# Kernel tuning notes

Measured on AMD Instinct MI355X. Metric: run time of the kernel, lower is better.

The kernel has to match this reference:

```python
import jax, jax.numpy as jnp
import numpy as np
import math

N_EMBD = 1024
N_HEAD = 16
HEAD_DIM = N_EMBD // N_HEAD
SEQ = 2048
BATCH = 2
EPS = 1e-5


def _gelu_tanh(x):
    c = math.sqrt(2.0 / math.pi)
    return 0.5 * x * (1.0 + jnp.tanh(c * (x + 0.044715 * x ** 3)))


def _layernorm(x, w, b):
    mean = jnp.mean(x, axis=-1, keepdims=True)
    var = jnp.mean(jnp.square(x - mean), axis=-1, keepdims=True)  # unbiased=False
    return (x - mean) / jnp.sqrt(var + EPS) * w + b


def setup_inputs() -> dict:
    key = jax.random.key(0)
    ks = jax.random.split(key, 8)
    D = N_EMBD
    s = 0.02
    return {
        "x": jax.random.normal(ks[0], (BATCH, SEQ, D), jnp.float32),
        "ln1_w": jnp.ones((D,), jnp.float32),
        "ln1_b": jnp.zeros((D,), jnp.float32),
        "w_qkv": jax.random.normal(ks[1], (D, 3 * D), jnp.float32) * s,
        "b_qkv": jnp.zeros((3 * D,), jnp.float32),
        "w_attn_proj": jax.random.normal(ks[2], (D, D), jnp.float32) * s,
        "b_attn_proj": jnp.zeros((D,), jnp.float32),
        "ln2_w": jnp.ones((D,), jnp.float32),
        "ln2_b": jnp.zeros((D,), jnp.float32),
        "w_fc": jax.random.normal(ks[3], (D, 4 * D), jnp.float32) * s,
        "b_fc": jnp.zeros((4 * D,), jnp.float32),
        "w_proj": jax.random.normal(ks[4], (4 * D, D), jnp.float32) * s,
        "b_proj": jnp.zeros((D,), jnp.float32),
    }


def reference(x, ln1_w, ln1_b, w_qkv, b_qkv, w_attn_proj, b_attn_proj,
              ln2_w, ln2_b, w_fc, b_fc, w_proj, b_proj):
    bs, T, D = x.shape
    # --- attention branch (pre-LN) ---
    h = _layernorm(x, ln1_w, ln1_b)
    qkv = h @ w_qkv + b_qkv                      # [B,T,3D]
    q, k, v = jnp.split(qkv, 3, axis=-1)
    q = q.reshape(bs, T, N_HEAD, HEAD_DIM).transpose(0, 2, 1, 3)  # [B,H,T,d]
    k = k.reshape(bs, T, N_HEAD, HEAD_DIM).transpose(0, 2, 1, 3)
    v = v.reshape(bs, T, N_HEAD, HEAD_DIM).transpose(0, 2, 1, 3)
    scores = jnp.einsum("bhqd,bhkd->bhqk", q, k) * (1.0 / math.sqrt(HEAD_DIM))
    causal = jnp.tril(jnp.ones((T, T), bool))
    scores = jnp.where(causal[None, None], scores, -jnp.inf)
    att = jax.nn.softmax(scores, axis=-1)
    ctx = jnp.einsum("bhqk,bhkd->bhqd", att, v)
    ctx = ctx.transpose(0, 2, 1, 3).reshape(bs, T, D)
    attn_out = ctx @ w_attn_proj + b_attn_proj
    x = x + attn_out
    # --- MLP branch (pre-LN) ---
    h = _layernorm(x, ln2_w, ln2_b)
    h = _gelu_tanh(h @ w_fc + b_fc)
    h = h @ w_proj + b_proj
    return x + h
```

## Files before the change

kernel.cpp:

```cpp
#include <hip/hip_runtime.h>

typedef unsigned short u16;
typedef __attribute__((ext_vector_type(8))) __bf16 bf16x8;
typedef __attribute__((ext_vector_type(8))) unsigned short ushort8;
typedef __attribute__((ext_vector_type(4))) float f32x4;

#define MFMA16(a, b, c) __builtin_amdgcn_mfma_f32_16x16x32_bf16((a), (b), (c), 0, 0, 0)

__device__ __forceinline__ u16 f2bf(float f) {
  union { float f; unsigned u; } v; v.f = f;
  unsigned r = v.u + 0x7fffu + ((v.u >> 16) & 1u);
  return (u16)(r >> 16);
}

__device__ __forceinline__ void async16(const u16* g, u16* l) {
  __builtin_amdgcn_global_load_lds(
      (const __attribute__((address_space(1))) void*)g,
      (__attribute__((address_space(3))) void*)l, 16, 0, 0);
}

__global__ __launch_bounds__(256)
void transpose_bf16(const float* __restrict__ W, u16* __restrict__ Wt, int K, int N) {
  __shared__ float t[32][33];
  const int n0 = blockIdx.x * 32, k0 = blockIdx.y * 32;
  const int tx = threadIdx.x, ty = threadIdx.y;
  #pragma unroll
  for (int i = 0; i < 32; i += 8)
    t[ty + i][tx] = W[(size_t)(k0 + ty + i) * N + n0 + tx];
  __syncthreads();
  #pragma unroll
  for (int i = 0; i < 32; i += 8)
    Wt[(size_t)(n0 + ty + i) * K + k0 + tx] = f2bf(t[tx][ty + i]);
}

__global__ __launch_bounds__(256)
void transpose_v(const u16* __restrict__ v, u16* __restrict__ vt) {
  __shared__ u16 t[64][72];
  const int bh = blockIdx.y, t0 = blockIdx.x * 64;
  const int tid = threadIdx.x;
  #pragma unroll
  for (int s = 0; s < 2; ++s) {
    const int idx = tid + s * 256;
    const int row = idx >> 3, ch = idx & 7;
    ushort8 d = *(const ushort8*)(v + ((size_t)bh * 2048 + t0 + row) * 64 + ch * 8);
    #pragma unroll
    for (int e = 0; e < 8; ++e) t[ch * 8 + e][row] = d[e];
  }
  __syncthreads();
  #pragma unroll
  for (int s = 0; s < 2; ++s) {
    const int idx = tid + s * 256;
    const int drow = idx >> 3, ch = idx & 7;
    ushort8 o = *(const ushort8*)(&t[drow][ch * 8]);
    *(ushort8*)(vt + ((size_t)bh * 64 + drow) * 2048 + t0 + ch * 8) = o;
  }
}

__global__ __launch_bounds__(256)
void ln_bf16(const float* __restrict__ X, const float* __restrict__ w,
             const float* __restrict__ bia, u16* __restrict__ out) {
  const int row = blockIdx.x, tid = threadIdx.x;
  const float4 v = ((const float4*)(X + (size_t)row * 1024))[tid];
  float s = v.x + v.y + v.z + v.w;
  float s2 = v.x * v.x + v.y * v.y + v.z * v.z + v.w * v.w;
  #pragma unroll
  for (int o = 32; o > 0; o >>= 1) { s += __shfl_down(s, o); s2 += __shfl_down(s2, o); }
  __shared__ float red[8];
  const int wv = tid >> 6, lane = tid & 63;
  if (lane == 0) { red[wv] = s; red[4 + wv] = s2; }
  __syncthreads();
  s = red[0] + red[1] + red[2] + red[3];
  s2 = red[4] + red[5] + red[6] + red[7];
  const float mean = s * (1.f / 1024.f);
  const float var = s2 * (1.f / 1024.f) - mean * mean;
  const float rstd = rsqrtf(var + 1e-5f);
  const float4 wv4 = ((const float4*)w)[tid];
  const float4 bv4 = ((const float4*)bia)[tid];
  ushort4 o;
  o.x = f2bf((v.x - mean) * rstd * wv4.x + bv4.x);
  o.y = f2bf((v.y - mean) * rstd * wv4.y + bv4.y);
  o.z = f2bf((v.z - mean) * rstd * wv4.z + bv4.z);
  o.w = f2bf((v.w - mean) * rstd * wv4.w + bv4.w);
  ((ushort4*)(out + (size_t)row * 1024))[tid] = o;
}

template <int MODE>
__global__ __launch_bounds__(256)
void gemm_bt(const u16* __restrict__ A, const u16* __restrict__ Bt,
             const float* __restrict__ bias, const float* __restrict__ resid,
             float* __restrict__ outF, u16* __restrict__ outB,
             u16* __restrict__ qo, u16* __restrict__ ko, u16* __restrict__ vo,
             int M, int N, int K, int kSlice) {
  __shared__ u16 As[128 * 64];
  __shared__ u16 Bs[128 * 64];
  const int tid = threadIdx.x;
  const int lane = tid & 63, wv = tid >> 6;
  const int l16 = lane & 15, quad = lane >> 4;
  const int wr = wv >> 1, wc = wv & 1;
  const int m0 = blockIdx.y * 128, n0 = blockIdx.x * 128;
  const int kBegin = blockIdx.z * kSlice, kEnd = kBegin + kSlice;
  const int srow = lane >> 3;
  const int sch = (lane & 7) ^ srow;

  f32x4 acc[4][4];
  const f32x4 fz = {0.f, 0.f, 0.f, 0.f};
  #pragma unroll
  for (int i = 0; i < 4; ++i)
    #pragma unroll
    for (int j = 0; j < 4; ++j) acc[i][j] = fz;

  for (int k0 = kBegin; k0 < kEnd; k0 += 64) {
    __syncthreads();
    #pragma unroll
    for (int s = 0; s < 4; ++s) {
      const int R = wv * 32 + s * 8;
      async16(A + (size_t)(m0 + R + srow) * K + k0 + sch * 8, As + R * 64);
      async16(Bt + (size_t)(n0 + R + srow) * K + k0 + sch * 8, Bs + R * 64);
    }
    __builtin_amdgcn_s_waitcnt(0xF70);
    __syncthreads();
    #pragma unroll
    for (int h = 0; h < 2; ++h) {
      bf16x8 af[4], bfr[4];
      #pragma unroll
      for (int i = 0; i < 4; ++i) {
        const int row = wr * 64 + i * 16 + l16;
        af[i] = *(const bf16x8*)(As + row * 64 + (((h * 4 + quad) ^ (l16 & 7)) * 8));
      }
      #pragma unroll
      for (int j = 0; j < 4; ++j) {
        const int row = wc * 64 + j * 16 + l16;
        bfr[j] = *(const bf16x8*)(Bs + row * 64 + (((h * 4 + quad) ^ (l16 & 7)) * 8));
      }
      #pragma unroll
      for (int i = 0; i < 4; ++i)
        #pragma unroll
        for (int j = 0; j < 4; ++j)
          acc[i][j] = MFMA16(af[i], bfr[j], acc[i][j]);
    }
  }

  #pragma unroll
  for (int i = 0; i < 4; ++i) {
    #pragma unroll
    for (int j = 0; j < 4; ++j) {
      const int col = n0 + wc * 64 + j * 16 + l16;
      const float bc = bias[col];
      #pragma unroll
      for (int r = 0; r < 4; ++r) {
        const int row = m0 + wr * 64 + i * 16 + quad * 4 + r;
        float v = acc[i][j][r];
        if (MODE != 4) v += bc;
        if (MODE == 0) {
          const int which = col >> 10, cc = col & 1023, hh = cc >> 6, dd = cc & 63;
          const int bb = row >> 11, t = row & 2047;
          const u16 bv = f2bf(v);
          const size_t o = ((size_t)(bb * 16 + hh) * 2048 + t) * 64 + dd;
          if (which == 0)
            qo[o] = bv;
          else if (which == 1)
            ko[o] = bv;
          else
            vo[o] = bv;
        } else if (MODE == 1) {
          outF[(size_t)row * N + col] = resid[(size_t)row * N + col] + v;
        } else if (MODE == 2) {
          const float x3 = v * v * v;
          const float u = 0.7978845608028654f * (v + 0.044715f * x3);
          const float e = __expf(2.f * u);
          const float th = 1.f - 2.f / (e + 1.f);
          outB[(size_t)row * N + col] = f2bf(0.5f * v * (1.f + th));
        } else {
          outF[(size_t)blockIdx.z * M * N + (size_t)row * N + col] = v;
        }
      }
    }
  }
}

__global__ __launch_bounds__(256)
void reduce2(const float* __restrict__ P, const float* __restrict__ resid,
             const float* __restrict__ bias, float* __restrict__ out, int MN, int N) {
  const int idx4 = blockIdx.x * 256 + threadIdx.x;
  const size_t s = (size_t)MN >> 2;
  const float4 a = ((const float4*)P)[idx4];
  const float4 b = ((const float4*)P)[idx4 + s];
  const float4 r = ((const float4*)resid)[idx4];
  const float4 bb = ((const float4*)bias)[idx4 & (N / 4 - 1)];
  float4 o;
  o.x = r.x + a.x + b.x + bb.x;
  o.y = r.y + a.y + b.y + bb.y;
  o.z = r.z + a.z + b.z + bb.z;
  o.w = r.w + a.w + b.w + bb.w;
  ((float4*)out)[idx4] = o;
}

__global__ __launch_bounds__(256)
void attn(const u16* __restrict__ Q, const u16* __restrict__ Kg,
          const u16* __restrict__ Vt, u16* __restrict__ ctx) {
  __shared__ u16 Ks[128 * 64];
  __shared__ u16 Vs[64 * 128];
  __shared__ u16 Ps[64 * 128];
  const int px = blockIdx.x;
  const int pair = px >> 1, half = px & 1;
  const int qt0 = pair, qt1 = 15 - pair;
  const int bh = blockIdx.y;
  const int b = bh >> 4, h = bh & 15;
  const int tid = threadIdx.x;
  const int lane = tid & 63, wv = tid >> 6;
  const int l16 = lane & 15, quad = lane >> 4;
  const int rb = half * 64 + wv * 16;
  const u16* Qb = Q + (size_t)bh * 2048 * 64;
  const u16* Kb = Kg + (size_t)bh * 2048 * 64;
  const u16* Vb = Vt + (size_t)bh * 64 * 2048;

  bf16x8 qf[2][2];
  #pragma unroll
  for (int t = 0; t < 2; ++t)
    #pragma unroll
    for (int c = 0; c < 2; ++c)
      qf[t][c] = *(const bf16x8*)(Qb + (size_t)((t ? qt1 : qt0) * 128 + rb + l16) * 64 +
                                  c * 32 + quad * 8);

  f32x4 octx[2][4];
  const f32x4 fz = {0.f, 0.f, 0.f, 0.f};
  #pragma unroll
  for (int t = 0; t < 2; ++t)
    #pragma unroll
    for (int jd = 0; jd < 4; ++jd) octx[t][jd] = fz;
  float mi[2][4], li[2][4];
  #pragma unroll
  for (int t = 0; t < 2; ++t)
    #pragma unroll
    for (int r = 0; r < 4; ++r) { mi[t][r] = -1e30f; li[t][r] = 0.f; }

  for (int kt = 0; kt <= qt1; ++kt) {
    __syncthreads();
    #pragma unroll
    for (int s = 0; s < 4; ++s) {
      const int cid = tid + s * 256;
      {
        const int key = cid >> 3, ch = cid & 7;
        ushort8 d = *(const ushort8*)(Kb + (size_t)(kt * 128 + key) * 64 + ch * 8);
        *(ushort8*)(Ks + key * 64 + ((ch ^ (key & 7)) * 8)) = d;
      }
      {
        const int dd = cid >> 4, ch = cid & 15;
        ushort8 d = *(const ushort8*)(Vb + (size_t)dd * 2048 + kt * 128 + ch * 8);
        *(ushort8*)(Vs + dd * 128 + ((ch ^ (dd & 15)) * 8)) = d;
      }
    }
    __syncthreads();

    #pragma unroll
    for (int t = 0; t < 2; ++t) {
      const int qt = t ? qt1 : qt0;
      if (kt > qt) continue;

      f32x4 sa[8];
      #pragma unroll
      for (int j = 0; j < 8; ++j) {
        const int key7 = l16 & 7;
        bf16x8 kf0 = *(const bf16x8*)(Ks + (16 * j + l16) * 64 + ((quad ^ key7) * 8));
        bf16x8 kf1 = *(const bf16x8*)(Ks + (16 * j + l16) * 64 + (((4 + quad) ^ key7) * 8));
        f32x4 tt = MFMA16(qf[t][0], kf0, fz);
        sa[j] = MFMA16(qf[t][1], kf1, tt);
      }
      if (kt == qt) {
        #pragma unroll
        for (int j = 0; j < 8; ++j)
          #pragma unroll
          for (int r = 0; r < 4; ++r) {
            const int rg = rb + quad * 4 + r;
            const int cg = j * 16 + l16;
            if (cg > rg) sa[j][r] = -1e30f;
          }
      }
      #pragma unroll
      for (int r = 0; r < 4; ++r) {
        float mx = -1e30f;
        #pragma unroll
        for (int j = 0; j < 8; ++j) mx = fmaxf(mx, sa[j][r]);
        mx = fmaxf(mx, __shfl_xor(mx, 1));
        mx = fmaxf(mx, __shfl_xor(mx, 2));
        mx = fmaxf(mx, __shfl_xor(mx, 4));
        mx = fmaxf(mx, __shfl_xor(mx, 8));
        mx *= 0.125f;
        const float mn = fmaxf(mi[t][r], mx);
        const float al = __expf(mi[t][r] - mn);
        mi[t][r] = mn;
        const int row = wv * 16 + quad * 4 + r;
        const int rl = row & 15;
        float rs = 0.f;
        #pragma unroll
        for (int j = 0; j < 8; ++j) {
          const float p = __expf(sa[j][r] * 0.125f - mn);
          rs += p;
          const int colc = 2 * j + (l16 >> 3);
          Ps[row * 128 + ((colc ^ rl) * 8) + (l16 & 7)] = f2bf(p);
        }
        rs += __shfl_xor(rs, 1);
        rs += __shfl_xor(rs, 2);
        rs += __shfl_xor(rs, 4);
        rs += __shfl_xor(rs, 8);
        li[t][r] = li[t][r] * al + rs;
        #pragma unroll
        for (int jd = 0; jd < 4; ++jd) octx[t][jd][r] *= al;
      }
      #pragma unroll
      for (int c = 0; c < 4; ++c) {
        const int row = wv * 16 + l16;
        bf16x8 pf = *(const bf16x8*)(Ps + row * 128 + (((c * 4 + quad) ^ l16) * 8));
        #pragma unroll
        for (int jd = 0; jd < 4; ++jd) {
          const int dd = jd * 16 + l16;
          bf16x8 vf = *(const bf16x8*)(Vs + dd * 128 + (((c * 4 + quad) ^ (dd & 15)) * 8));
          octx[t][jd] = MFMA16(pf, vf, octx[t][jd]);
        }
      }
    }
  }
  #pragma unroll
  for (int t = 0; t < 2; ++t) {
    const int qt = t ? qt1 : qt0;
    #pragma unroll
    for (int jd = 0; jd < 4; ++jd)
      #pragma unroll
      for (int r = 0; r < 4; ++r) {
        const int rowg = qt * 128 + rb + quad * 4 + r;
        const int col = h * 64 + jd * 16 + l16;
        ctx[((size_t)b * 2048 + rowg) * 1024 + col] = f2bf(octx[t][jd][r] / li[t][r]);
      }
  }
}

extern "C" void kernel_launch(void* const* d_in, const int* in_sizes, int n_in,
                              void* d_out, int out_size, void* d_ws, size_t ws_size,
                              hipStream_t stream) {
  (void)in_sizes; (void)n_in; (void)out_size; (void)ws_size;
  const float* x      = (const float*)d_in[0];
  const float* ln1_w  = (const float*)d_in[1];
  const float* ln1_b  = (const float*)d_in[2];
  const float* w_qkv  = (const float*)d_in[3];
  const float* b_qkv  = (const float*)d_in[4];
  const float* w_attn = (const float*)d_in[5];
  const float* b_attn = (const float*)d_in[6];
  const float* ln2_w  = (const float*)d_in[7];
  const float* ln2_b  = (const float*)d_in[8];
  const float* w_fc   = (const float*)d_in[9];
  const float* b_fc   = (const float*)d_in[10];
  const float* w_proj = (const float*)d_in[11];
  const float* b_proj = (const float*)d_in[12];
  float* out = (float*)d_out;

  char* ws = (char*)d_ws;
  size_t off = 0;
  auto alloc = [&](size_t n) {
    char* p = ws + off;
    off += (n + 255) & ~(size_t)255;
    return p;
  };
  u16* h1     = (u16*)alloc(4096ull * 1024 * 2);
  u16* wqkvT  = (u16*)alloc(3072ull * 1024 * 2);
  u16* wattnT = (u16*)alloc(1024ull * 1024 * 2);
  u16* wfcT   = (u16*)alloc(4096ull * 1024 * 2);
  u16* wprojT = (u16*)alloc(1024ull * 4096 * 2);
  u16* q      = (u16*)alloc(4096ull * 1024 * 2);
  u16* k      = (u16*)alloc(4096ull * 1024 * 2);
  u16* vT     = (u16*)alloc(4096ull * 1024 * 2);
  u16* ctxb   = (u16*)alloc(4096ull * 1024 * 2);
  float* out1 = (float*)alloc(4096ull * 1024 * 4);
  u16* h2     = (u16*)alloc(4096ull * 1024 * 2);
  u16* fco    = (u16*)alloc(4096ull * 4096 * 2);

  u16* vtmp = ctxb;
  float* projP = (float*)q;

  const dim3 tb(32, 8);
  transpose_bf16<<<dim3(3072 / 32, 1024 / 32), tb, 0, stream>>>(w_qkv, wqkvT, 1024, 3072);
  transpose_bf16<<<dim3(1024 / 32, 1024 / 32), tb, 0, stream>>>(w_attn, wattnT, 1024, 1024);
  transpose_bf16<<<dim3(4096 / 32, 1024 / 32), tb, 0, stream>>>(w_fc, wfcT, 1024, 4096);
  transpose_bf16<<<dim3(1024 / 32, 4096 / 32), tb, 0, stream>>>(w_proj, wprojT, 4096, 1024);

  ln_bf16<<<4096, 256, 0, stream>>>(x, ln1_w, ln1_b, h1);

  gemm_bt<0><<<dim3(24, 32, 1), 256, 0, stream>>>(h1, wqkvT, b_qkv, nullptr, nullptr,
                                                  nullptr, q, k, vtmp, 4096, 3072, 1024, 1024);

  transpose_v<<<dim3(32, 32), 256, 0, stream>>>(vtmp, vT);

  attn<<<dim3(16, 32), 256, 0, stream>>>(q, k, vT, ctxb);

  gemm_bt<1><<<dim3(8, 32, 1), 256, 0, stream>>>(ctxb, wattnT, b_attn, x, out1, nullptr,
                                                 nullptr, nullptr, nullptr, 4096, 1024, 1024, 1024);

  ln_bf16<<<4096, 256, 0, stream>>>(out1, ln2_w, ln2_b, h2);

  gemm_bt<2><<<dim3(32, 32, 1), 256, 0, stream>>>(h2, wfcT, b_fc, nullptr, nullptr, fco,
                                                  nullptr, nullptr, nullptr, 4096, 4096, 1024, 1024);

  gemm_bt<4><<<dim3(8, 32, 2), 256, 0, stream>>>(fco, wprojT, b_proj, nullptr, projP, nullptr,
                                                 nullptr, nullptr, nullptr, 4096, 1024, 4096, 2048);

  reduce2<<<4096, 256, 0, stream>>>(projP, out1, b_proj, out, 4096 * 1024, 1024);
}
```

Baseline: 383.8 us.

## Transpose QK^T MFMA in attention to make softmax row-local per lane

Swaps the MFMA operands for the score computation so each lane holds one query row across 32 keys. The row max and sum then need only two cross-quad shuffles instead of four per row, and P is written to LDS as packed 4-element stores. Softmax switches to exp2 with a prescaled log2e constant, the final normalization uses a reciprocal, and f2bf now uses a hardware bf16 conversion. These cut ALU, shuffle and LDS store overhead at the cost of extra shuffles to redistribute alpha and l back to the output layout.

```diff
diff --git a/kernel.cpp b/kernel.cpp
--- a/kernel.cpp
+++ b/kernel.cpp
@@ -8,9 +8,9 @@
 #define MFMA16(a, b, c) __builtin_amdgcn_mfma_f32_16x16x32_bf16((a), (b), (c), 0, 0, 0)
 
 __device__ __forceinline__ u16 f2bf(float f) {
-  union { float f; unsigned u; } v; v.f = f;
-  unsigned r = v.u + 0x7fffu + ((v.u >> 16) & 1u);
-  return (u16)(r >> 16);
+  union { __bf16 h; u16 u; } cv;
+  cv.h = (__bf16)f;
+  return cv.u;
 }
 
 __device__ __forceinline__ void async16(const u16* g, u16* l) {
@@ -210,6 +210,7 @@
   const int lane = tid & 63, wv = tid >> 6;
   const int l16 = lane & 15, quad = lane >> 4;
   const int rb = half * 64 + wv * 16;
+  const float S2 = 0.18033688011112042f;
   const u16* Qb = Q + (size_t)bh * 2048 * 64;
   const u16* Kb = Kg + (size_t)bh * 2048 * 64;
   const u16* Vb = Vt + (size_t)bh * 64 * 2048;
@@ -228,11 +229,8 @@
   for (int t = 0; t < 2; ++t)
     #pragma unroll
     for (int jd = 0; jd < 4; ++jd) octx[t][jd] = fz;
-  float mi[2][4], li[2][4];
-  #pragma unroll
-  for (int t = 0; t < 2; ++t)
-    #pragma unroll
-    for (int r = 0; r < 4; ++r) { mi[t][r] = -1e30f; li[t][r] = 0.f; }
+  float mi2[2] = {-1e30f, -1e30f};
+  float li[2] = {0.f, 0.f};
 
   for (int kt = 0; kt <= qt1; ++kt) {
     __syncthreads();
@@ -263,54 +261,54 @@
         const int key7 = l16 & 7;
         bf16x8 kf0 = *(const bf16x8*)(Ks + (16 * j + l16) * 64 + ((quad ^ key7) * 8));
         bf16x8 kf1 = *(const bf16x8*)(Ks + (16 * j + l16) * 64 + (((4 + quad) ^ key7) * 8));
-        f32x4 tt = MFMA16(qf[t][0], kf0, fz);
-        sa[j] = MFMA16(qf[t][1], kf1, tt);
+        f32x4 tt = MFMA16(kf0, qf[t][0], fz);
+        sa[j] = MFMA16(kf1, qf[t][1], tt);
       }
       if (kt == qt) {
+        const int rg = rb + l16;
         #pragma unroll
         for (int j = 0; j < 8; ++j)
           #pragma unroll
-          for (int r = 0; r < 4; ++r) {
-            const int rg = rb + quad * 4 + r;
-            const int cg = j * 16 + l16;
-            if (cg > rg) sa[j][r] = -1e30f;
-          }
-      }
+          for (int r = 0; r < 4; ++r)
+            if (j * 16 + quad * 4 + r > rg) sa[j][r] = -1e30f;
+      }
+      float mx = -1e30f;
+      #pragma unroll
+      for (int j = 0; j < 8; ++j)
+        #pragma unroll
+        for (int r = 0; r < 4; ++r) mx = fmaxf(mx, sa[j][r]);
+      mx = fmaxf(mx, __shfl_xor(mx, 16));
+      mx = fmaxf(mx, __shfl_xor(mx, 32));
+      mx *= S2;
+      const float mn = fmaxf(mi2[t], mx);
+      const float al = __builtin_amdgcn_exp2f(mi2[t] - mn);
+      mi2[t] = mn;
+      const int row_local = wv * 16 + l16;
+      float rs = 0.f;
+      #pragma unroll
+      for (int j = 0; j < 8; ++j) {
+        ushort4 w4;
+        float p0 = __builtin_amdgcn_exp2f(sa[j][0] * S2 - mn);
+        float p1 = __builtin_amdgcn_exp2f(sa[j][1] * S2 - mn);
+        float p2 = __builtin_amdgcn_exp2f(sa[j][2] * S2 - mn);
+        float p3 = __builtin_amdgcn_exp2f(sa[j][3] * S2 - mn);
+        rs += (p0 + p1) + (p2 + p3);
+        w4.x = f2bf(p0); w4.y = f2bf(p1); w4.z = f2bf(p2); w4.w = f2bf(p3);
+        const int c = 2 * j + (quad >> 1);
+        *(ushort4*)(Ps + row_local * 128 + ((c ^ l16) * 8) + (quad & 1) * 4) = w4;
+      }
+      rs += __shfl_xor(rs, 16);
+      rs += __shfl_xor(rs, 32);
+      li[t] = li[t] * al + rs;
       #pragma unroll
       for (int r = 0; r < 4; ++r) {
-        float mx = -1e30f;
+        const float alr = __shfl(al, quad * 4 + r);
         #pragma unroll
-        for (int j = 0; j < 8; ++j) mx = fmaxf(mx, sa[j][r]);
-        mx = fmaxf(mx, __shfl_xor(mx, 1));
-        mx = fmaxf(mx, __shfl_xor(mx, 2));
-        mx = fmaxf(mx, __shfl_xor(mx, 4));
-        mx = fmaxf(mx, __shfl_xor(mx, 8));
-        mx *= 0.125f;
-        const float mn = fmaxf(mi[t][r], mx);
-        const float al = __expf(mi[t][r] - mn);
-        mi[t][r] = mn;
-        const int row = wv * 16 + quad * 4 + r;
-        const int rl = row & 15;
-        float rs = 0.f;
-        #pragma unroll
-        for (int j = 0; j < 8; ++j) {
-          const float p = __expf(sa[j][r] * 0.125f - mn);
-          rs += p;
-          const int colc = 2 * j + (l16 >> 3);
-          Ps[row * 128 + ((colc ^ rl) * 8) + (l16 & 7)] = f2bf(p);
-        }
-        rs += __shfl_xor(rs, 1);
-        rs += __shfl_xor(rs, 2);
-        rs += __shfl_xor(rs, 4);
-        rs += __shfl_xor(rs, 8);
-        li[t][r] = li[t][r] * al + rs;
-        #pragma unroll
-        for (int jd = 0; jd < 4; ++jd) octx[t][jd][r] *= al;
+        for (int jd = 0; jd < 4; ++jd) octx[t][jd][r] *= alr;
       }
       #pragma unroll
       for (int c = 0; c < 4; ++c) {
-        const int row = wv * 16 + l16;
-        bf16x8 pf = *(const bf16x8*)(Ps + row * 128 + (((c * 4 + quad) ^ l16) * 8));
+        bf16x8 pf = *(const bf16x8*)(Ps + row_local * 128 + (((c * 4 + quad) ^ l16) * 8));
         #pragma unroll
         for (int jd = 0; jd < 4; ++jd) {
           const int dd = jd * 16 + l16;
@@ -324,13 +322,15 @@
   for (int t = 0; t < 2; ++t) {
     const int qt = t ? qt1 : qt0;
     #pragma unroll
-    for (int jd = 0; jd < 4; ++jd)
-      #pragma unroll
-      for (int r = 0; r < 4; ++r) {
-        const int rowg = qt * 128 + rb + quad * 4 + r;
+    for (int r = 0; r < 4; ++r) {
+      const float lr = __builtin_amdgcn_rcpf(__shfl(li[t], quad * 4 + r));
+      const int rowg = qt * 128 + rb + quad * 4 + r;
+      #pragma unroll
+      for (int jd = 0; jd < 4; ++jd) {
         const int col = h * 64 + jd * 16 + l16;
-        ctx[((size_t)b * 2048 + rowg) * 1024 + col] = f2bf(octx[t][jd][r] / li[t][r]);
-      }
+        ctx[((size_t)b * 2048 + rowg) * 1024 + col] = f2bf(octx[t][jd][r] * lr);
+      }
+    }
   }
 }
 
```

Measured after the change: 373.7 us. 1.03x faster.

## Use async global-to-LDS loads in attention and split-K the attention projection

Applied to the files above, without the earlier changes.

The attention kernel now stages K and V tiles with direct global-to-LDS async loads instead of going through registers. The swizzle moves into the per-lane global source address while each wave writes a contiguous LDS block. The attention output projection drops the fused residual epilogue and runs as a two-way split-K GEMM into scratch, followed by the existing reduce2 kernel. This adds more blocks for the small GEMM at the cost of extra fp32 traffic. The bf16 conversion also switches to the native __bf16 cast, which may use hardware conversion instructions.

```diff
diff --git a/kernel.cpp b/kernel.cpp
--- a/kernel.cpp
+++ b/kernel.cpp
@@ -8,9 +8,9 @@
 #define MFMA16(a, b, c) __builtin_amdgcn_mfma_f32_16x16x32_bf16((a), (b), (c), 0, 0, 0)
 
 __device__ __forceinline__ u16 f2bf(float f) {
-  union { float f; unsigned u; } v; v.f = f;
-  unsigned r = v.u + 0x7fffu + ((v.u >> 16) & 1u);
-  return (u16)(r >> 16);
+  union { __bf16 h; u16 u; } cv;
+  cv.h = (__bf16)f;
+  return cv.u;
 }
 
 __device__ __forceinline__ void async16(const u16* g, u16* l) {
@@ -162,8 +162,6 @@
             ko[o] = bv;
           else
             vo[o] = bv;
-        } else if (MODE == 1) {
-          outF[(size_t)row * N + col] = resid[(size_t)row * N + col] + v;
         } else if (MODE == 2) {
           const float x3 = v * v * v;
           const float u = 0.7978845608028654f * (v + 0.044715f * x3);
@@ -214,6 +212,10 @@
   const u16* Kb = Kg + (size_t)bh * 2048 * 64;
   const u16* Vb = Vt + (size_t)bh * 64 * 2048;
 
+  const int kRow = lane >> 3;
+  const int kCh = (lane & 7) ^ (kRow & 7);
+  const int vRow = lane >> 4;
+
   bf16x8 qf[2][2];
   #pragma unroll
   for (int t = 0; t < 2; ++t)
@@ -238,18 +240,17 @@
     __syncthreads();
     #pragma unroll
     for (int s = 0; s < 4; ++s) {
-      const int cid = tid + s * 256;
-      {
-        const int key = cid >> 3, ch = cid & 7;
-        ushort8 d = *(const ushort8*)(Kb + (size_t)(kt * 128 + key) * 64 + ch * 8);
-        *(ushort8*)(Ks + key * 64 + ((ch ^ (key & 7)) * 8)) = d;
-      }
-      {
-        const int dd = cid >> 4, ch = cid & 15;
-        ushort8 d = *(const ushort8*)(Vb + (size_t)dd * 2048 + kt * 128 + ch * 8);
-        *(ushort8*)(Vs + dd * 128 + ((ch ^ (dd & 15)) * 8)) = d;
-      }
-    }
+      const int R = wv * 32 + s * 8;
+      async16(Kb + (size_t)(kt * 128 + R + kRow) * 64 + kCh * 8, Ks + R * 64);
+    }
+    #pragma unroll
+    for (int s = 0; s < 4; ++s) {
+      const int D = wv * 16 + s * 4;
+      const int dd = D + vRow;
+      const int sch = (lane & 15) ^ (dd & 15);
+      async16(Vb + (size_t)dd * 2048 + kt * 128 + sch * 8, Vs + D * 128);
+    }
+    __builtin_amdgcn_s_waitcnt(0xF70);
     __syncthreads();
 
     #pragma unroll
@@ -374,6 +375,7 @@
   u16* fco    = (u16*)alloc(4096ull * 4096 * 2);
 
   u16* vtmp = ctxb;
+  float* apP = (float*)fco;
   float* projP = (float*)q;
 
   const dim3 tb(32, 8);
@@ -391,8 +393,9 @@
 
   attn<<<dim3(16, 32), 256, 0, stream>>>(q, k, vT, ctxb);
 
-  gemm_bt<1><<<dim3(8, 32, 1), 256, 0, stream>>>(ctxb, wattnT, b_attn, x, out1, nullptr,
-                                                 nullptr, nullptr, nullptr, 4096, 1024, 1024, 1024);
+  gemm_bt<4><<<dim3(8, 32, 2), 256, 0, stream>>>(ctxb, wattnT, b_attn, nullptr, apP, nullptr,
+                                                 nullptr, nullptr, nullptr, 4096, 1024, 1024, 512);
+  reduce2<<<4096, 256, 0, stream>>>(apP, x, b_attn, out1, 4096 * 1024, 1024);
 
   ln_bf16<<<4096, 256, 0, stream>>>(out1, ln2_w, ln2_b, h2);
 
```

Result: no change. 379.4 us (-1.1%).
